# Kernel optimization log

Measured on AMD Instinct MI355X. Metric: run time of the kernel, lower is better.

The kernel has to match this reference:

```python
import jax, jax.numpy as jnp
import numpy as np

D_MODEL = 1024
N_HEADS = 16
HEAD_DIM = D_MODEL // N_HEADS


def setup_inputs() -> dict:
    key = jax.random.key(0)
    ks = jax.random.split(key, 5)
    s = 1.0 / np.sqrt(D_MODEL)
    return {
        "x": jax.random.normal(ks[0], (2, 2048, D_MODEL), dtype=jnp.float32),
        "w_qkv": jax.random.uniform(ks[1], (3 * D_MODEL, D_MODEL), jnp.float32, -s, s),
        "b_qkv": jax.random.uniform(ks[2], (3 * D_MODEL,), jnp.float32, -s, s),
        "w_out": jax.random.uniform(ks[3], (D_MODEL, D_MODEL), jnp.float32, -s, s),
        "b_out": jax.random.uniform(ks[4], (D_MODEL,), jnp.float32, -s, s),
    }


def _attn(x, w_qkv, b_qkv, w_out, b_out):
    bsz, seq_len, _ = x.shape
    qkv = jnp.einsum('bsd,ed->bse', x, w_qkv) + b_qkv  # [B,S,3D]
    q, k, v = jnp.split(qkv, 3, axis=-1)
    def heads(t):  # [B,S,D] -> [B,H,S,Dh]
        return t.reshape(bsz, seq_len, N_HEADS, HEAD_DIM).transpose(0, 2, 1, 3)
    q, k, v = heads(q), heads(k), heads(v)
    scores = jnp.einsum('bhqd,bhkd->bhqk', q, k) / np.sqrt(HEAD_DIM)
    mask = jnp.tril(jnp.ones((seq_len, seq_len), dtype=bool))
    scores = jnp.where(mask, scores, -jnp.inf)
    probs = jax.nn.softmax(scores, axis=-1)
    attn = jnp.einsum('bhqk,bhkd->bhqd', probs, v)
    attn = attn.transpose(0, 2, 1, 3).reshape(bsz, seq_len, D_MODEL)
    return jnp.einsum('bsd,ed->bse', attn, w_out) + b_out


def reference(x, w_qkv, b_qkv, w_out, b_out):
    return _attn(x, w_qkv, b_qkv, w_out, b_out)
```

## Files before the change

kernel.cpp:

```cpp
#include <hip/hip_runtime.h>
#include <hip/hip_bf16.h>
#include <stdint.h>

#define SEQ     2048
#define BATCH   2
#define NHEADS  16
#define HDIM    64
#define DMODEL  1024
#define N3      3072
#define D2      2048
#define MTOT    (BATCH*SEQ)

typedef __attribute__((ext_vector_type(4))) float f32x4;
typedef __attribute__((ext_vector_type(8))) short bf16x8;

static __device__ inline unsigned short f2bf(float f) {
    union { float f; unsigned u; } v; v.f = f;
    unsigned r = (v.u + 0x7fffu + ((v.u >> 16) & 1u)) >> 16;
    return (unsigned short)r;
}
static __device__ inline unsigned pk2bf(float a, float b) {
    union { __hip_bfloat162 h; unsigned u; } c;
    c.h = __float22bfloat162_rn(make_float2(a, b));
    return c.u;
}

#define GLDS(gp, lp) __builtin_amdgcn_global_load_lds( \
    (const __attribute__((address_space(1))) void*)(gp), \
    (__attribute__((address_space(3))) void*)(lp), 16, 0, 0)

__global__ void cast_all(const float* __restrict__ x,
                         const float* __restrict__ wqkv,
                         const float* __restrict__ wout,
                         unsigned short* __restrict__ xb,
                         unsigned short* __restrict__ wqkvb,
                         unsigned short* __restrict__ woutb) {
    long i4 = (long)(blockIdx.x * blockDim.x + threadIdx.x) * 4;
    const float* src; unsigned short* dst; long off;
    if (i4 < 4194304L)      { src = x;    dst = xb;    off = i4; }
    else if (i4 < 7340032L) { src = wqkv; dst = wqkvb; off = i4 - 4194304L; }
    else                    { src = wout; dst = woutb; off = i4 - 7340032L; }
    float4 v = *(const float4*)(src + off);
    union { uint2 u; ushort4 s; } pk;
    pk.u.x = pk2bf(v.x, v.y); pk.u.y = pk2bf(v.z, v.w);
    *(ushort4*)(dst + off) = pk.s;
}

__global__ __launch_bounds__(512, 1) void gemm_qkv(
    const unsigned short* __restrict__ A,
    const unsigned short* __restrict__ B,
    const float* __restrict__ bias,
    unsigned short* __restrict__ qk,
    unsigned short* __restrict__ vT)
{
    __shared__ __align__(16) unsigned short sA[2][256][64];
    __shared__ __align__(16) unsigned short sB[2][256][64];
    const int tid  = threadIdx.x;
    const int w    = tid >> 6, lane = tid & 63;
    const int quad = lane >> 4, l16 = lane & 15, l7 = l16 & 7;
    const int wm = w >> 2, wn = w & 3;
    const int bid = blockIdx.x;
    const int m0 = (bid & 15) << 8;
    const int n0 = (bid >> 4) << 8;

    f32x4 acc[8][4];
    const f32x4 zero = {0.f, 0.f, 0.f, 0.f};
    #pragma unroll
    for (int i = 0; i < 8; i++)
        #pragma unroll
        for (int j = 0; j < 4; j++) acc[i][j] = zero;

    const int rsel = tid >> 3;
    const int sgl  = (tid & 7) ^ (rsel & 7);
    const unsigned short* gA = A + (long)(m0 + rsel) * 1024 + sgl * 8;
    const unsigned short* gB = B + (long)(n0 + rsel) * 1024 + sgl * 8;
    const int srow = w * 8;

    bf16x8 af[4][2];
    bf16x8 bfr[2][2][2];

    auto stageA = [&](int nb, int h, long ko) {
        GLDS(gA + (long)(h * 128)      * 1024 + ko, &sA[nb][h * 128 +      srow][0]);
        GLDS(gA + (long)(h * 128 + 64) * 1024 + ko, &sA[nb][h * 128 + 64 + srow][0]);
    };
    auto stageB = [&](int nb, int h, long ko) {
        GLDS(gB + (long)(h * 128)      * 1024 + ko, &sB[nb][h * 128 +      srow][0]);
        GLDS(gB + (long)(h * 128 + 64) * 1024 + ko, &sB[nb][h * 128 + 64 + srow][0]);
    };
    auto loadA = [&](int c, int mh) {
        #pragma unroll
        for (int mt2 = 0; mt2 < 4; mt2++)
            #pragma unroll
            for (int kk = 0; kk < 2; kk++)
                af[mt2][kk] = *(const bf16x8*)(
                    &sA[c][mh * 128 + wm * 64 + mt2 * 16 + l16]
                          [(((kk << 2) + quad) ^ l7) * 8]);
    };
    auto loadB = [&](int c, int nh) {
        #pragma unroll
        for (int nt2 = 0; nt2 < 2; nt2++)
            #pragma unroll
            for (int kk = 0; kk < 2; kk++)
                bfr[nh][nt2][kk] = *(const bf16x8*)(
                    &sB[c][nh * 128 + wn * 32 + nt2 * 16 + l16]
                          [(((kk << 2) + quad) ^ l7) * 8]);
    };
    auto mfmaQ = [&](int mh, int nh) {
        __builtin_amdgcn_s_setprio(1);
        #pragma unroll
        for (int mt2 = 0; mt2 < 4; mt2++)
            #pragma unroll
            for (int nt2 = 0; nt2 < 2; nt2++)
                #pragma unroll
                for (int kk = 0; kk < 2; kk++)
                    acc[mh * 4 + mt2][nh * 2 + nt2] =
                        __builtin_amdgcn_mfma_f32_16x16x32_bf16(
                            af[mt2][kk], bfr[nh][nt2][kk],
                            acc[mh * 4 + mt2][nh * 2 + nt2], 0, 0, 0);
        __builtin_amdgcn_s_setprio(0);
    };

    stageB(0, 0, 0); stageB(0, 1, 0); stageA(0, 0, 0); stageA(0, 1, 0);
    __builtin_amdgcn_sched_barrier(0);
    asm volatile("s_waitcnt vmcnt(2)" ::: "memory");
    __builtin_amdgcn_sched_barrier(0);
    __builtin_amdgcn_s_barrier();

    for (int t = 0; t < 15; ++t) {
        const int c = t & 1, nb = c ^ 1;
        const long ko = (long)(t + 1) * 64;

        loadA(c, 0); loadB(c, 0);
        stageB(nb, 0, ko);
        __builtin_amdgcn_s_barrier();
        asm volatile("s_waitcnt lgkmcnt(0)" ::: "memory");
        __builtin_amdgcn_sched_barrier(0);
        mfmaQ(0, 0);
        __builtin_amdgcn_sched_barrier(0);
        __builtin_amdgcn_s_barrier();

        loadB(c, 1);
        stageB(nb, 1, ko);
        __builtin_amdgcn_sched_barrier(0);
        asm volatile("s_waitcnt vmcnt(4)" ::: "memory");
        __builtin_amdgcn_sched_barrier(0);
        __builtin_amdgcn_s_barrier();
        asm volatile("s_waitcnt lgkmcnt(0)" ::: "memory");
        __builtin_amdgcn_sched_barrier(0);
        mfmaQ(0, 1);
        __builtin_amdgcn_sched_barrier(0);
        __builtin_amdgcn_s_barrier();

        loadA(c, 1);
        stageA(nb, 0, ko);
        __builtin_amdgcn_s_barrier();
        asm volatile("s_waitcnt lgkmcnt(0)" ::: "memory");
        __builtin_amdgcn_sched_barrier(0);
        mfmaQ(1, 1);
        __builtin_amdgcn_sched_barrier(0);
        __builtin_amdgcn_s_barrier();

        stageA(nb, 1, ko);
        __builtin_amdgcn_sched_barrier(0);
        asm volatile("s_waitcnt vmcnt(2)" ::: "memory");
        __builtin_amdgcn_sched_barrier(0);
        __builtin_amdgcn_s_barrier();
        mfmaQ(1, 0);
        __builtin_amdgcn_sched_barrier(0);
        __builtin_amdgcn_s_barrier();
    }
    {
        const int c = 1;
        loadA(c, 0); loadB(c, 0);
        __builtin_amdgcn_s_barrier();
        asm volatile("s_waitcnt lgkmcnt(0)" ::: "memory");
        __builtin_amdgcn_sched_barrier(0);
        mfmaQ(0, 0);
        __builtin_amdgcn_sched_barrier(0);
        __builtin_amdgcn_s_barrier();

        loadB(c, 1);
        __builtin_amdgcn_sched_barrier(0);
        asm volatile("s_waitcnt vmcnt(0)" ::: "memory");
        __builtin_amdgcn_sched_barrier(0);
        __builtin_amdgcn_s_barrier();
        asm volatile("s_waitcnt lgkmcnt(0)" ::: "memory");
        __builtin_amdgcn_sched_barrier(0);
        mfmaQ(0, 1);
        __builtin_amdgcn_sched_barrier(0);
        __builtin_amdgcn_s_barrier();

        loadA(c, 1);
        __builtin_amdgcn_s_barrier();
        asm volatile("s_waitcnt lgkmcnt(0)" ::: "memory");
        __builtin_amdgcn_sched_barrier(0);
        mfmaQ(1, 1);
        mfmaQ(1, 0);
    }

    if (n0 < 2048) {
        #pragma unroll
        for (int ni = 0; ni < 4; ni++) {
            const int n_g = n0 + (ni >> 1) * 128 + wn * 32 + (ni & 1) * 16 + l16;
            const float bv = bias[n_g];
            #pragma unroll
            for (int mi = 0; mi < 8; mi++) {
                const int mb = (mi >> 2) * 128 + wm * 64 + (mi & 3) * 16 + quad * 4;
                #pragma unroll
                for (int r = 0; r < 4; r++) {
                    const int m_g = m0 + mb + r;
                    qk[(long)m_g * D2 + n_g] = f2bf(acc[mi][ni][r] + bv);
                }
            }
        }
    } else {
        const int b = m0 >> 11;
        #pragma unroll
        for (int ni = 0; ni < 4; ni++) {
            const int n_g = n0 + (ni >> 1) * 128 + wn * 32 + (ni & 1) * 16 + l16;
            const int dm = n_g - 2048;
            const long vrow = (long)(((b << 4) + (dm >> 6)) << 6) + (dm & 63);
            const float bv = bias[n_g];
            #pragma unroll
            for (int mi = 0; mi < 8; mi++) {
                const int m_g = m0 + (mi >> 2) * 128 + wm * 64 + (mi & 3) * 16 + quad * 4;
                union { uint2 u; ushort4 s; } pk;
                pk.u.x = pk2bf(acc[mi][ni][0] + bv, acc[mi][ni][1] + bv);
                pk.u.y = pk2bf(acc[mi][ni][2] + bv, acc[mi][ni][3] + bv);
                *(ushort4*)(vT + vrow * D2 + (m_g & 2047)) = pk.s;
            }
        }
    }
}

__global__ __launch_bounds__(256, 2) void gemm_out(
    const unsigned short* __restrict__ A,
    const unsigned short* __restrict__ B,
    const float* __restrict__ bias,
    float* __restrict__ C)
{
    __shared__ __align__(16) unsigned short sA[2][128][64];
    __shared__ __align__(16) unsigned short sB[2][64][64];
    const int tid  = threadIdx.x;
    const int wave = tid >> 6, lane = tid & 63;
    const int quad = lane >> 4, l16 = lane & 15, l7 = l16 & 7;
    const int wm = wave >> 1, wn = wave & 1;
    const int m0 = blockIdx.x * 128, n0 = blockIdx.y * 64;

    f32x4 acc[4][2];
    const f32x4 zero = {0.f, 0.f, 0.f, 0.f};
    #pragma unroll
    for (int i = 0; i < 4; i++) { acc[i][0] = zero; acc[i][1] = zero; }

    const int rsel = tid >> 3;
    const int sgl  = (tid & 7) ^ (rsel & 7);
    const unsigned short* gA0 = A + (long)(m0 + rsel) * 1024 + sgl * 8;
    const unsigned short* gB0 = B + (long)(n0 + rsel) * 1024 + sgl * 8;

    #pragma unroll
    for (int i = 0; i < 4; i++)
        GLDS(gA0 + (long)(32 * i) * 1024, &sA[0][32 * i + wave * 8][0]);
    #pragma unroll
    for (int i = 0; i < 2; i++)
        GLDS(gB0 + (long)(32 * i) * 1024, &sB[0][32 * i + wave * 8][0]);

    int buf = 0;
    for (int k0 = 0; k0 < 1024; k0 += 64, buf ^= 1) {
        __syncthreads();
        if (k0 + 64 < 1024) {
            #pragma unroll
            for (int i = 0; i < 4; i++)
                GLDS(gA0 + (long)(32 * i) * 1024 + k0 + 64, &sA[buf ^ 1][32 * i + wave * 8][0]);
            #pragma unroll
            for (int i = 0; i < 2; i++)
                GLDS(gB0 + (long)(32 * i) * 1024 + k0 + 64, &sB[buf ^ 1][32 * i + wave * 8][0]);
        }
        #pragma unroll
        for (int ks = 0; ks < 2; ks++) {
            bf16x8 af[4], bfr[2];
            #pragma unroll
            for (int mt = 0; mt < 4; mt++)
                af[mt] = *(const bf16x8*)(&sA[buf][wm * 64 + mt * 16 + l16][((ks * 4 + quad) ^ l7) * 8]);
            #pragma unroll
            for (int nt = 0; nt < 2; nt++)
                bfr[nt] = *(const bf16x8*)(&sB[buf][wn * 32 + nt * 16 + l16][((ks * 4 + quad) ^ l7) * 8]);
            #pragma unroll
            for (int mt = 0; mt < 4; mt++)
                #pragma unroll
                for (int nt = 0; nt < 2; nt++)
                    acc[mt][nt] = __builtin_amdgcn_mfma_f32_16x16x32_bf16(
                        af[mt], bfr[nt], acc[mt][nt], 0, 0, 0);
        }
    }
    #pragma unroll
    for (int nt = 0; nt < 2; nt++) {
        const int n_g = n0 + wn * 32 + nt * 16 + l16;
        const float bv = bias[n_g];
        #pragma unroll
        for (int mt = 0; mt < 4; mt++) {
            #pragma unroll
            for (int r = 0; r < 4; r++) {
                const int m_g = m0 + wm * 64 + mt * 16 + quad * 4 + r;
                C[(long)m_g * DMODEL + n_g] = acc[mt][nt][r] + bv;
            }
        }
    }
}

__global__ __launch_bounds__(512, 1) void attn_kernel(
    const unsigned short* __restrict__ qk,
    const unsigned short* __restrict__ vT,
    unsigned short* __restrict__ attn)
{
    __shared__ __align__(16) unsigned short sK [2][2][64][64];
    __shared__ __align__(16) unsigned short sVt[2][2][64][64];
    __shared__ __align__(16) unsigned short sP [8][16][64];

    const int tid  = threadIdx.x;
    const int w    = tid >> 6, lane = tid & 63;
    const int quad = lane >> 4, l16 = lane & 15, l7 = l16 & 7;

    const int bh = blockIdx.x;
    const int b  = bh >> 4, h = bh & 15;
    const int pair = blockIdx.y;
    const long rowb = (long)b * SEQ;

    const int rl = lane >> 3;
    const int sm = (lane & 7) ^ rl;
    const unsigned short* kg = qk + (rowb + w * 8 + rl) * D2 + 1024 + h * HDIM + sm * 8;
    const unsigned short* vg = vT + (long)(bh * 64 + w * 8 + rl) * D2 + sm * 8;

    const int s0 = quad ^ l7;
    const float C2 = 0.18033688011112042f;
    const f32x4 zero = {0.f, 0.f, 0.f, 0.f};

    #pragma unroll
    for (int ph = 0; ph < 2; ph++) {
        const int qtile  = ph ? (15 - pair) : pair;
        const int qbase  = qtile * 128;
        const int ntiles = 2 * qtile + 2;
        const int npairs = ntiles >> 1;

        bf16x8 qf0, qf1;
        {
            const unsigned short* qp = qk + (rowb + qbase + w * 16 + l16) * D2 + h * HDIM;
            qf0 = *(const bf16x8*)(qp + quad * 8);
            qf1 = *(const bf16x8*)(qp + 32 + quad * 8);
        }
        f32x4 Oacc[4];
        #pragma unroll
        for (int mf = 0; mf < 4; mf++) Oacc[mf] = zero;
        float l_i = 0.f;

        __syncthreads();
        {
            GLDS(kg,            &sK [0][0][w * 8][0]);
            GLDS(vg,            &sVt[0][0][w * 8][0]);
            GLDS(kg + 64L * D2, &sK [0][1][w * 8][0]);
            GLDS(vg + 64,       &sVt[0][1][w * 8][0]);
        }

        int buf = 0;
        for (int p = 0; p < npairs; p++, buf ^= 1) {
            __syncthreads();
            if (p + 1 < npairs) {
                const long o0 = (long)(2 * p + 2) * 64;
                const long o1 = (long)(2 * p + 3) * 64;
                GLDS(kg + o0 * D2, &sK [buf ^ 1][0][w * 8][0]);
                GLDS(vg + o0,      &sVt[buf ^ 1][0][w * 8][0]);
                GLDS(kg + o1 * D2, &sK [buf ^ 1][1][w * 8][0]);
                GLDS(vg + o1,      &sVt[buf ^ 1][1][w * 8][0]);
            }
            #pragma unroll
            for (int s = 0; s < 2; s++) {
                const int t = 2 * p + s;

                f32x4 st[4];
                __builtin_amdgcn_s_setprio(1);
                #pragma unroll
                for (int kvf = 0; kvf < 4; kvf++) {
                    bf16x8 kf0 = *(const bf16x8*)(&sK[buf][s][kvf * 16 + l16][s0 * 8]);
                    bf16x8 kf1 = *(const bf16x8*)(&sK[buf][s][kvf * 16 + l16][(s0 ^ 4) * 8]);
                    st[kvf] = __builtin_amdgcn_mfma_f32_16x16x32_bf16(kf0, qf0, zero, 0, 0, 0);
                    st[kvf] = __builtin_amdgcn_mfma_f32_16x16x32_bf16(kf1, qf1, st[kvf], 0, 0, 0);
                }
                __builtin_amdgcn_s_setprio(0);
                if (t >= 2 * qtile) {
                    const int ql = w * 16 + l16;
                    const int tb = (t - 2 * qtile) * 64;
                    #pragma unroll
                    for (int kvf = 0; kvf < 4; kvf++) {
                        const int kv = tb + kvf * 16 + quad * 4;
                        #pragma unroll
                        for (int r = 0; r < 4; r++)
                            if (kv + r > ql) st[kvf][r] = -1e30f;
                    }
                }
                #pragma unroll
                for (int kvf = 0; kvf < 4; kvf++) {
                    #pragma unroll
                    for (int r = 0; r < 4; r++)
                        st[kvf][r] = __builtin_amdgcn_exp2f(st[kvf][r] * C2);
                }
                f32x4 ps = (st[0] + st[1]) + (st[2] + st[3]);
                l_i += (ps[0] + ps[1]) + (ps[2] + ps[3]);

                #pragma unroll
                for (int kvf = 0; kvf < 4; kvf++) {
                    union { uint2 u; ushort4 s4; } pk;
                    pk.u.x = pk2bf(st[kvf][0], st[kvf][1]);
                    pk.u.y = pk2bf(st[kvf][2], st[kvf][3]);
                    const int seg = (kvf * 2 + (quad >> 1)) ^ l7;
                    *(ushort4*)(&sP[w][l16][seg * 8 + (quad & 1) * 4]) = pk.s4;
                }
                bf16x8 pf0 = *(const bf16x8*)(&sP[w][l16][(quad ^ l7) * 8]);
                bf16x8 pf1 = *(const bf16x8*)(&sP[w][l16][((4 + quad) ^ l7) * 8]);
                __builtin_amdgcn_s_setprio(1);
                #pragma unroll
                for (int mf = 0; mf < 4; mf++) {
                    bf16x8 vf0 = *(const bf16x8*)(&sVt[buf][s][mf * 16 + l16][s0 * 8]);
                    bf16x8 vf1 = *(const bf16x8*)(&sVt[buf][s][mf * 16 + l16][(s0 ^ 4) * 8]);
                    Oacc[mf] = __builtin_amdgcn_mfma_f32_16x16x32_bf16(vf0, pf0, Oacc[mf], 0, 0, 0);
                    Oacc[mf] = __builtin_amdgcn_mfma_f32_16x16x32_bf16(vf1, pf1, Oacc[mf], 0, 0, 0);
                }
                __builtin_amdgcn_s_setprio(0);
            }
        }
        float L = l_i;
        L += __shfl_xor(L, 16);
        L += __shfl_xor(L, 32);
        const float inv = 1.0f / L;
        const int q = qbase + w * 16 + l16;
        unsigned short* op = attn + (rowb + q) * DMODEL + h * HDIM + quad * 4;
        #pragma unroll
        for (int mf = 0; mf < 4; mf++) {
            union { uint2 u; ushort4 s4; } pk;
            pk.u.x = pk2bf(Oacc[mf][0] * inv, Oacc[mf][1] * inv);
            pk.u.y = pk2bf(Oacc[mf][2] * inv, Oacc[mf][3] * inv);
            *(ushort4*)(op + mf * 16) = pk.s4;
        }
    }
}

extern "C" void kernel_launch(void* const* d_in, const int* in_sizes, int n_in,
                              void* d_out, int out_size, void* d_ws, size_t ws_size,
                              hipStream_t stream) {
    const float* x    = (const float*)d_in[0];
    const float* wqkv = (const float*)d_in[1];
    const float* bqkv = (const float*)d_in[2];
    const float* wout = (const float*)d_in[3];
    const float* bout = (const float*)d_in[4];

    char* ws = (char*)d_ws;
    unsigned short* xb    = (unsigned short*)(ws);
    unsigned short* wqkvb = (unsigned short*)(ws + (8L << 20));
    unsigned short* woutb = (unsigned short*)(ws + (14L << 20));
    unsigned short* qkb   = (unsigned short*)(ws + (16L << 20));
    unsigned short* vTb   = (unsigned short*)(ws + (32L << 20));
    unsigned short* attnb = (unsigned short*)(ws + (40L << 20));

    cast_all<<<8192, 256, 0, stream>>>(x, wqkv, wout, xb, wqkvb, woutb);

    gemm_qkv<<<192, 512, 0, stream>>>(xb, wqkvb, bqkv, qkb, vTb);

    dim3 g2(32, 8);
    attn_kernel<<<g2, 512, 0, stream>>>(qkb, vTb, attnb);

    dim3 g3(32, 16);
    gemm_out<<<g3, 256, 0, stream>>>(attnb, woutb, bout, (float*)d_out);
}
```

Measured before the change: 171.4 us.

## Fuse cast, QKV GEMM, attention and output GEMM into one cooperative kernel

```diff
diff --git a/kernel.cpp b/kernel.cpp
--- a/kernel.cpp
+++ b/kernel.cpp
@@ -1,6 +1,9 @@
 #include <hip/hip_runtime.h>
 #include <hip/hip_bf16.h>
+#include <hip/hip_cooperative_groups.h>
 #include <stdint.h>
+
+namespace cg = cooperative_groups;
 
 #define SEQ     2048
 #define BATCH   2
@@ -29,415 +32,411 @@
     (const __attribute__((address_space(1))) void*)(gp), \
     (__attribute__((address_space(3))) void*)(lp), 16, 0, 0)
 
-__global__ void cast_all(const float* __restrict__ x,
-                         const float* __restrict__ wqkv,
-                         const float* __restrict__ wout,
-                         unsigned short* __restrict__ xb,
-                         unsigned short* __restrict__ wqkvb,
-                         unsigned short* __restrict__ woutb) {
-    long i4 = (long)(blockIdx.x * blockDim.x + threadIdx.x) * 4;
-    const float* src; unsigned short* dst; long off;
-    if (i4 < 4194304L)      { src = x;    dst = xb;    off = i4; }
-    else if (i4 < 7340032L) { src = wqkv; dst = wqkvb; off = i4 - 4194304L; }
-    else                    { src = wout; dst = woutb; off = i4 - 7340032L; }
-    float4 v = *(const float4*)(src + off);
-    union { uint2 u; ushort4 s; } pk;
-    pk.u.x = pk2bf(v.x, v.y); pk.u.y = pk2bf(v.z, v.w);
-    *(ushort4*)(dst + off) = pk.s;
-}
-
-__global__ __launch_bounds__(512, 1) void gemm_qkv(
-    const unsigned short* __restrict__ A,
-    const unsigned short* __restrict__ B,
-    const float* __restrict__ bias,
+__global__ __launch_bounds__(512, 1) void fused(
+    const float* __restrict__ x,
+    const float* __restrict__ wqkv,
+    const float* __restrict__ bqkv,
+    const float* __restrict__ wout,
+    const float* __restrict__ bout,
+    unsigned short* __restrict__ xb,
+    unsigned short* __restrict__ wqkvb,
+    unsigned short* __restrict__ woutb,
     unsigned short* __restrict__ qk,
-    unsigned short* __restrict__ vT)
+    unsigned short* __restrict__ vT,
+    unsigned short* __restrict__ attnb,
+    float* __restrict__ out)
 {
-    __shared__ __align__(16) unsigned short sA[2][256][64];
-    __shared__ __align__(16) unsigned short sB[2][256][64];
-    const int tid  = threadIdx.x;
+    __shared__ __align__(16) char smem[131072];
+    const int vb  = blockIdx.x;
+    const int tid = threadIdx.x;
     const int w    = tid >> 6, lane = tid & 63;
     const int quad = lane >> 4, l16 = lane & 15, l7 = l16 & 7;
-    const int wm = w >> 2, wn = w & 3;
-    const int bid = blockIdx.x;
-    const int m0 = (bid & 15) << 8;
-    const int n0 = (bid >> 4) << 8;
-
-    f32x4 acc[8][4];
+    cg::grid_group grid = cg::this_grid();
     const f32x4 zero = {0.f, 0.f, 0.f, 0.f};
-    #pragma unroll
-    for (int i = 0; i < 8; i++)
+
+    {
+        const long gid = (long)vb * 512 + tid;
+        for (int p = 0; p < 16; p++) {
+            long i4 = (p * 131072L + gid) * 4;
+            const float* src; unsigned short* dst; long off;
+            if (i4 < 4194304L)      { src = x;    dst = xb;    off = i4; }
+            else if (i4 < 7340032L) { src = wqkv; dst = wqkvb; off = i4 - 4194304L; }
+            else                    { src = wout; dst = woutb; off = i4 - 7340032L; }
+            float4 v = *(const float4*)(src + off);
+            union { uint2 u; ushort4 s; } pk;
+            pk.u.x = pk2bf(v.x, v.y); pk.u.y = pk2bf(v.z, v.w);
+            *(ushort4*)(dst + off) = pk.s;
+        }
+    }
+    __threadfence();
+    grid.sync();
+
+    if (vb < 192) {
+        unsigned short (*sA)[256][64] = (unsigned short (*)[256][64])(smem);
+        unsigned short (*sB)[256][64] = (unsigned short (*)[256][64])(smem + 65536);
+        const int wm = w >> 2, wn = w & 3;
+        const int m0 = (vb & 15) << 8;
+        const int n0 = (vb >> 4) << 8;
+
+        f32x4 acc[8][4];
         #pragma unroll
-        for (int j = 0; j < 4; j++) acc[i][j] = zero;
-
-    const int rsel = tid >> 3;
-    const int sgl  = (tid & 7) ^ (rsel & 7);
-    const unsigned short* gA = A + (long)(m0 + rsel) * 1024 + sgl * 8;
-    const unsigned short* gB = B + (long)(n0 + rsel) * 1024 + sgl * 8;
-    const int srow = w * 8;
-
-    bf16x8 af[4][2];
-    bf16x8 bfr[2][2][2];
-
-    auto stageA = [&](int nb, int h, long ko) {
-        GLDS(gA + (long)(h * 128)      * 1024 + ko, &sA[nb][h * 128 +      srow][0]);
-        GLDS(gA + (long)(h * 128 + 64) * 1024 + ko, &sA[nb][h * 128 + 64 + srow][0]);
-    };
-    auto stageB = [&](int nb, int h, long ko) {
-        GLDS(gB + (long)(h * 128)      * 1024 + ko, &sB[nb][h * 128 +      srow][0]);
-        GLDS(gB + (long)(h * 128 + 64) * 1024 + ko, &sB[nb][h * 128 + 64 + srow][0]);
-    };
-    auto loadA = [&](int c, int mh) {
-        #pragma unroll
-        for (int mt2 = 0; mt2 < 4; mt2++)
-            #pragma unroll
-            for (int kk = 0; kk < 2; kk++)
-                af[mt2][kk] = *(const bf16x8*)(
-                    &sA[c][mh * 128 + wm * 64 + mt2 * 16 + l16]
-                          [(((kk << 2) + quad) ^ l7) * 8]);
-    };
-    auto loadB = [&](int c, int nh) {
-        #pragma unroll
-        for (int nt2 = 0; nt2 < 2; nt2++)
-            #pragma unroll
-            for (int kk = 0; kk < 2; kk++)
-                bfr[nh][nt2][kk] = *(const bf16x8*)(
-                    &sB[c][nh * 128 + wn * 32 + nt2 * 16 + l16]
-                          [(((kk << 2) + quad) ^ l7) * 8]);
-    };
-    auto mfmaQ = [&](int mh, int nh) {
-        __builtin_amdgcn_s_setprio(1);
-        #pragma unroll
-        for (int mt2 = 0; mt2 < 4; mt2++)
+        for (int i = 0; i < 8; i++)
+            #pragma unroll
+            for (int j = 0; j < 4; j++) acc[i][j] = zero;
+
+        const int rsel = tid >> 3;
+        const int sgl  = (tid & 7) ^ (rsel & 7);
+        const unsigned short* gA = xb    + (long)(m0 + rsel) * 1024 + sgl * 8;
+        const unsigned short* gB = wqkvb + (long)(n0 + rsel) * 1024 + sgl * 8;
+        const int srow = w * 8;
+
+        bf16x8 af[4][2];
+        bf16x8 bfr[2][2][2];
+
+        auto stageA = [&](int nb, int h, long ko) {
+            GLDS(gA + (long)(h * 128)      * 1024 + ko, &sA[nb][h * 128 +      srow][0]);
+            GLDS(gA + (long)(h * 128 + 64) * 1024 + ko, &sA[nb][h * 128 + 64 + srow][0]);
+        };
+        auto stageB = [&](int nb, int h, long ko) {
+            GLDS(gB + (long)(h * 128)      * 1024 + ko, &sB[nb][h * 128 +      srow][0]);
+            GLDS(gB + (long)(h * 128 + 64) * 1024 + ko, &sB[nb][h * 128 + 64 + srow][0]);
+        };
+        auto loadA = [&](int c, int mh) {
+            #pragma unroll
+            for (int mt2 = 0; mt2 < 4; mt2++)
+                #pragma unroll
+                for (int kk = 0; kk < 2; kk++)
+                    af[mt2][kk] = *(const bf16x8*)(
+                        &sA[c][mh * 128 + wm * 64 + mt2 * 16 + l16]
+                              [(((kk << 2) + quad) ^ l7) * 8]);
+        };
+        auto loadB = [&](int c, int nh) {
             #pragma unroll
             for (int nt2 = 0; nt2 < 2; nt2++)
                 #pragma unroll
                 for (int kk = 0; kk < 2; kk++)
-                    acc[mh * 4 + mt2][nh * 2 + nt2] =
-                        __builtin_amdgcn_mfma_f32_16x16x32_bf16(
-                            af[mt2][kk], bfr[nh][nt2][kk],
-                            acc[mh * 4 + mt2][nh * 2 + nt2], 0, 0, 0);
-        __builtin_amdgcn_s_setprio(0);
-    };
-
-    stageB(0, 0, 0); stageB(0, 1, 0); stageA(0, 0, 0); stageA(0, 1, 0);
-    __builtin_amdgcn_sched_barrier(0);
-    asm volatile("s_waitcnt vmcnt(2)" ::: "memory");
-    __builtin_amdgcn_sched_barrier(0);
-    __builtin_amdgcn_s_barrier();
-
-    for (int t = 0; t < 15; ++t) {
-        const int c = t & 1, nb = c ^ 1;
-        const long ko = (long)(t + 1) * 64;
-
-        loadA(c, 0); loadB(c, 0);
-        stageB(nb, 0, ko);
-        __builtin_amdgcn_s_barrier();
-        asm volatile("s_waitcnt lgkmcnt(0)" ::: "memory");
-        __builtin_amdgcn_sched_barrier(0);
-        mfmaQ(0, 0);
-        __builtin_amdgcn_sched_barrier(0);
-        __builtin_amdgcn_s_barrier();
-
-        loadB(c, 1);
-        stageB(nb, 1, ko);
-        __builtin_amdgcn_sched_barrier(0);
-        asm volatile("s_waitcnt vmcnt(4)" ::: "memory");
-        __builtin_amdgcn_sched_barrier(0);
-        __builtin_amdgcn_s_barrier();
-        asm volatile("s_waitcnt lgkmcnt(0)" ::: "memory");
-        __builtin_amdgcn_sched_barrier(0);
-        mfmaQ(0, 1);
-        __builtin_amdgcn_sched_barrier(0);
-        __builtin_amdgcn_s_barrier();
-
-        loadA(c, 1);
-        stageA(nb, 0, ko);
-        __builtin_amdgcn_s_barrier();
-        asm volatile("s_waitcnt lgkmcnt(0)" ::: "memory");
-        __builtin_amdgcn_sched_barrier(0);
-        mfmaQ(1, 1);
-        __builtin_amdgcn_sched_barrier(0);
-        __builtin_amdgcn_s_barrier();
-
-        stageA(nb, 1, ko);
+                    bfr[nh][nt2][kk] = *(const bf16x8*)(
+                        &sB[c][nh * 128 + wn * 32 + nt2 * 16 + l16]
+                              [(((kk << 2) + quad) ^ l7) * 8]);
+        };
+        auto mfmaQ = [&](int mh, int nh) {
+            __builtin_amdgcn_s_setprio(1);
+            #pragma unroll
+            for (int mt2 = 0; mt2 < 4; mt2++)
+                #pragma unroll
+                for (int nt2 = 0; nt2 < 2; nt2++)
+                    #pragma unroll
+                    for (int kk = 0; kk < 2; kk++)
+                        acc[mh * 4 + mt2][nh * 2 + nt2] =
+                            __builtin_amdgcn_mfma_f32_16x16x32_bf16(
+                                af[mt2][kk], bfr[nh][nt2][kk],
+                                acc[mh * 4 + mt2][nh * 2 + nt2], 0, 0, 0);
+            __builtin_amdgcn_s_setprio(0);
+        };
+
+        stageB(0, 0, 0); stageB(0, 1, 0); stageA(0, 0, 0); stageA(0, 1, 0);
         __builtin_amdgcn_sched_barrier(0);
         asm volatile("s_waitcnt vmcnt(2)" ::: "memory");
         __builtin_amdgcn_sched_barrier(0);
         __builtin_amdgcn_s_barrier();
-        mfmaQ(1, 0);
-        __builtin_amdgcn_sched_barrier(0);
-        __builtin_amdgcn_s_barrier();
+
+        for (int t = 0; t < 15; ++t) {
+            const int c = t & 1, nb = c ^ 1;
+            const long ko = (long)(t + 1) * 64;
+
+            loadA(c, 0); loadB(c, 0);
+            stageB(nb, 0, ko);
+            __builtin_amdgcn_s_barrier();
+            asm volatile("s_waitcnt lgkmcnt(0)" ::: "memory");
+            __builtin_amdgcn_sched_barrier(0);
+            mfmaQ(0, 0);
+            __builtin_amdgcn_sched_barrier(0);
+            __builtin_amdgcn_s_barrier();
+
+            loadB(c, 1);
+            stageB(nb, 1, ko);
+            __builtin_amdgcn_sched_barrier(0);
+            asm volatile("s_waitcnt vmcnt(4)" ::: "memory");
+            __builtin_amdgcn_sched_barrier(0);
+            __builtin_amdgcn_s_barrier();
+            asm volatile("s_waitcnt lgkmcnt(0)" ::: "memory");
+            __builtin_amdgcn_sched_barrier(0);
+            mfmaQ(0, 1);
+            __builtin_amdgcn_sched_barrier(0);
+            __builtin_amdgcn_s_barrier();
+
+            loadA(c, 1);
+            stageA(nb, 0, ko);
+            __builtin_amdgcn_s_barrier();
+            asm volatile("s_waitcnt lgkmcnt(0)" ::: "memory");
+            __builtin_amdgcn_sched_barrier(0);
+            mfmaQ(1, 1);
+            __builtin_amdgcn_sched_barrier(0);
+            __builtin_amdgcn_s_barrier();
+
+            stageA(nb, 1, ko);
+            __builtin_amdgcn_sched_barrier(0);
+            asm volatile("s_waitcnt vmcnt(2)" ::: "memory");
+            __builtin_amdgcn_sched_barrier(0);
+            __builtin_amdgcn_s_barrier();
+            mfmaQ(1, 0);
+            __builtin_amdgcn_sched_barrier(0);
+            __builtin_amdgcn_s_barrier();
+        }
+        {
+            const int c = 1;
+            loadA(c, 0); loadB(c, 0);
+            __builtin_amdgcn_s_barrier();
+            asm volatile("s_waitcnt lgkmcnt(0)" ::: "memory");
+            __builtin_amdgcn_sched_barrier(0);
+            mfmaQ(0, 0);
+            __builtin_amdgcn_sched_barrier(0);
+            __builtin_amdgcn_s_barrier();
+
+            loadB(c, 1);
+            __builtin_amdgcn_sched_barrier(0);
+            asm volatile("s_waitcnt vmcnt(0)" ::: "memory");
+            __builtin_amdgcn_sched_barrier(0);
+            __builtin_amdgcn_s_barrier();
+            asm volatile("s_waitcnt lgkmcnt(0)" ::: "memory");
+            __builtin_amdgcn_sched_barrier(0);
+            mfmaQ(0, 1);
+            __builtin_amdgcn_sched_barrier(0);
+            __builtin_amdgcn_s_barrier();
+
+            loadA(c, 1);
+            __builtin_amdgcn_s_barrier();
+            asm volatile("s_waitcnt lgkmcnt(0)" ::: "memory");
+            __builtin_amdgcn_sched_barrier(0);
+            mfmaQ(1, 1);
+            mfmaQ(1, 0);
+        }
+
+        if (n0 < 2048) {
+            #pragma unroll
+            for (int ni = 0; ni < 4; ni++) {
+                const int n_g = n0 + (ni >> 1) * 128 + wn * 32 + (ni & 1) * 16 + l16;
+                const float bv = bqkv[n_g];
+                #pragma unroll
+                for (int mi = 0; mi < 8; mi++) {
+                    const int mb = (mi >> 2) * 128 + wm * 64 + (mi & 3) * 16 + quad * 4;
+                    #pragma unroll
+                    for (int r = 0; r < 4; r++) {
+                        const int m_g = m0 + mb + r;
+                        qk[(long)m_g * D2 + n_g] = f2bf(acc[mi][ni][r] + bv);
+                    }
+                }
+            }
+        } else {
+            const int b = m0 >> 11;
+            #pragma unroll
+            for (int ni = 0; ni < 4; ni++) {
+                const int n_g = n0 + (ni >> 1) * 128 + wn * 32 + (ni & 1) * 16 + l16;
+                const int dm = n_g - 2048;
+                const long vrow = (long)(((b << 4) + (dm >> 6)) << 6) + (dm & 63);
+                const float bv = bqkv[n_g];
+                #pragma unroll
+                for (int mi = 0; mi < 8; mi++) {
+                    const int m_g = m0 + (mi >> 2) * 128 + wm * 64 + (mi & 3) * 16 + quad * 4;
+                    union { uint2 u; ushort4 s; } pk;
+                    pk.u.x = pk2bf(acc[mi][ni][0] + bv, acc[mi][ni][1] + bv);
+                    pk.u.y = pk2bf(acc[mi][ni][2] + bv, acc[mi][ni][3] + bv);
+                    *(ushort4*)(vT + vrow * D2 + (m_g & 2047)) = pk.s;
+                }
+            }
+        }
     }
+    __threadfence();
+    grid.sync();
+
     {
-        const int c = 1;
-        loadA(c, 0); loadB(c, 0);
-        __builtin_amdgcn_s_barrier();
-        asm volatile("s_waitcnt lgkmcnt(0)" ::: "memory");
-        __builtin_amdgcn_sched_barrier(0);
-        mfmaQ(0, 0);
-        __builtin_amdgcn_sched_barrier(0);
-        __builtin_amdgcn_s_barrier();
-
-        loadB(c, 1);
-        __builtin_amdgcn_sched_barrier(0);
-        asm volatile("s_waitcnt vmcnt(0)" ::: "memory");
-        __builtin_amdgcn_sched_barrier(0);
-        __builtin_amdgcn_s_barrier();
-        asm volatile("s_waitcnt lgkmcnt(0)" ::: "memory");
-        __builtin_amdgcn_sched_barrier(0);
-        mfmaQ(0, 1);
-        __builtin_amdgcn_sched_barrier(0);
-        __builtin_amdgcn_s_barrier();
-
-        loadA(c, 1);
-        __builtin_amdgcn_s_barrier();
-        asm volatile("s_waitcnt lgkmcnt(0)" ::: "memory");
-        __builtin_amdgcn_sched_barrier(0);
-        mfmaQ(1, 1);
-        mfmaQ(1, 0);
-    }
-
-    if (n0 < 2048) {
+        unsigned short (*sK)[2][64][64]  = (unsigned short (*)[2][64][64])(smem);
+        unsigned short (*sVt)[2][64][64] = (unsigned short (*)[2][64][64])(smem + 32768);
+        unsigned short (*sP)[16][64]     = (unsigned short (*)[16][64])(smem + 65536);
+
+        const int bh = vb >> 3;
+        const int b  = bh >> 4, h = bh & 15;
+        const int pair = vb & 7;
+        const long rowb = (long)b * SEQ;
+
+        const int rl = lane >> 3;
+        const int sm = (lane & 7) ^ rl;
+        const unsigned short* kg = qk + (rowb + w * 8 + rl) * D2 + 1024 + h * HDIM + sm * 8;
+        const unsigned short* vg = vT + (long)(bh * 64 + w * 8 + rl) * D2 + sm * 8;
+
+        const int s0 = quad ^ l7;
+        const float C2 = 0.18033688011112042f;
+
         #pragma unroll
-        for (int ni = 0; ni < 4; ni++) {
-            const int n_g = n0 + (ni >> 1) * 128 + wn * 32 + (ni & 1) * 16 + l16;
-            const float bv = bias[n_g];
-            #pragma unroll
-            for (int mi = 0; mi < 8; mi++) {
-                const int mb = (mi >> 2) * 128 + wm * 64 + (mi & 3) * 16 + quad * 4;
-                #pragma unroll
-                for (int r = 0; r < 4; r++) {
-                    const int m_g = m0 + mb + r;
-                    qk[(long)m_g * D2 + n_g] = f2bf(acc[mi][ni][r] + bv);
+        for (int ph = 0; ph < 2; ph++) {
+            const int qtile  = ph ? (15 - pair) : pair;
+            const int qbase  = qtile * 128;
+            const int ntiles = 2 * qtile + 2;
+            const int npairs = ntiles >> 1;
+
+            bf16x8 qf0, qf1;
+            {
+                const unsigned short* qp = qk + (rowb + qbase + w * 16 + l16) * D2 + h * HDIM;
+                qf0 = *(const bf16x8*)(qp + quad * 8);
+                qf1 = *(const bf16x8*)(qp + 32 + quad * 8);
+            }
+            f32x4 Oacc[4];
+            #pragma unroll
+            for (int mf = 0; mf < 4; mf++) Oacc[mf] = zero;
+            float l_i = 0.f;
+
+            __syncthreads();
+            {
+                GLDS(kg,            &sK [0][0][w * 8][0]);
+                GLDS(vg,            &sVt[0][0][w * 8][0]);
+                GLDS(kg + 64L * D2, &sK [0][1][w * 8][0]);
+                GLDS(vg + 64,       &sVt[0][1][w * 8][0]);
+            }
+
+            int buf = 0;
+            for (int p = 0; p < npairs; p++, buf ^= 1) {
+                __syncthreads();
+                if (p + 1 < npairs) {
+                    const long o0 = (long)(2 * p + 2) * 64;
+                    const long o1 = (long)(2 * p + 3) * 64;
+                    GLDS(kg + o0 * D2, &sK [buf ^ 1][0][w * 8][0]);
+                    GLDS(vg + o0,      &sVt[buf ^ 1][0][w * 8][0]);
+                    GLDS(kg + o1 * D2, &sK [buf ^ 1][1][w * 8][0]);
+                    GLDS(vg + o1,      &sVt[buf ^ 1][1][w * 8][0]);
                 }
-            }
-        }
-    } else {
-        const int b = m0 >> 11;
-        #pragma unroll
-        for (int ni = 0; ni < 4; ni++) {
-            const int n_g = n0 + (ni >> 1) * 128 + wn * 32 + (ni & 1) * 16 + l16;
-            const int dm = n_g - 2048;
-            const long vrow = (long)(((b << 4) + (dm >> 6)) << 6) + (dm & 63);
-            const float bv = bias[n_g];
-            #pragma unroll
-            for (int mi = 0; mi < 8; mi++) {
-                const int m_g = m0 + (mi >> 2) * 128 + wm * 64 + (mi & 3) * 16 + quad * 4;
-                union { uint2 u; ushort4 s; } pk;
-                pk.u.x = pk2bf(acc[mi][ni][0] + bv, acc[mi][ni][1] + bv);
-                pk.u.y = pk2bf(acc[mi][ni][2] + bv, acc[mi][ni][3] + bv);
-                *(ushort4*)(vT + vrow * D2 + (m_g & 2047)) = pk.s;
-            }
-        }
-    }
-}
-
-__global__ __launch_bounds__(256, 2) void gemm_out(
-    const unsigned short* __restrict__ A,
-    const unsigned short* __restrict__ B,
-    const float* __restrict__ bias,
-    float* __restrict__ C)
-{
-    __shared__ __align__(16) unsigned short sA[2][128][64];
-    __shared__ __align__(16) unsigned short sB[2][64][64];
-    const int tid  = threadIdx.x;
-    const int wave = tid >> 6, lane = tid & 63;
-    const int quad = lane >> 4, l16 = lane & 15, l7 = l16 & 7;
-    const int wm = wave >> 1, wn = wave & 1;
-    const int m0 = blockIdx.x * 128, n0 = blockIdx.y * 64;
-
-    f32x4 acc[4][2];
-    const f32x4 zero = {0.f, 0.f, 0.f, 0.f};
-    #pragma unroll
-    for (int i = 0; i < 4; i++) { acc[i][0] = zero; acc[i][1] = zero; }
-
-    const int rsel = tid >> 3;
-    const int sgl  = (tid & 7) ^ (rsel & 7);
-    const unsigned short* gA0 = A + (long)(m0 + rsel) * 1024 + sgl * 8;
-    const unsigned short* gB0 = B + (long)(n0 + rsel) * 1024 + sgl * 8;
-
-    #pragma unroll
-    for (int i = 0; i < 4; i++)
-        GLDS(gA0 + (long)(32 * i) * 1024, &sA[0][32 * i + wave * 8][0]);
-    #pragma unroll
-    for (int i = 0; i < 2; i++)
-        GLDS(gB0 + (long)(32 * i) * 1024, &sB[0][32 * i + wave * 8][0]);
-
-    int buf = 0;
-    for (int k0 = 0; k0 < 1024; k0 += 64, buf ^= 1) {
-        __syncthreads();
-        if (k0 + 64 < 1024) {
-            #pragma unroll
-            for (int i = 0; i < 4; i++)
-                GLDS(gA0 + (long)(32 * i) * 1024 + k0 + 64, &sA[buf ^ 1][32 * i + wave * 8][0]);
-            #pragma unroll
-            for (int i = 0; i < 2; i++)
-                GLDS(gB0 + (long)(32 * i) * 1024 + k0 + 64, &sB[buf ^ 1][32 * i + wave * 8][0]);
-        }
-        #pragma unroll
-        for (int ks = 0; ks < 2; ks++) {
-            bf16x8 af[4], bfr[2];
-            #pragma unroll
-            for (int mt = 0; mt < 4; mt++)
-                af[mt] = *(const bf16x8*)(&sA[buf][wm * 64 + mt * 16 + l16][((ks * 4 + quad) ^ l7) * 8]);
-            #pragma unroll
-            for (int nt = 0; nt < 2; nt++)
-                bfr[nt] = *(const bf16x8*)(&sB[buf][wn * 32 + nt * 16 + l16][((ks * 4 + quad) ^ l7) * 8]);
-            #pragma unroll
-            for (int mt = 0; mt < 4; mt++)
-                #pragma unroll
-                for (int nt = 0; nt < 2; nt++)
-                    acc[mt][nt] = __builtin_amdgcn_mfma_f32_16x16x32_bf16(
-                        af[mt], bfr[nt], acc[mt][nt], 0, 0, 0);
-        }
-    }
-    #pragma unroll
-    for (int nt = 0; nt < 2; nt++) {
-        const int n_g = n0 + wn * 32 + nt * 16 + l16;
-        const float bv = bias[n_g];
-        #pragma unroll
-        for (int mt = 0; mt < 4; mt++) {
-            #pragma unroll
-            for (int r = 0; r < 4; r++) {
-                const int m_g = m0 + wm * 64 + mt * 16 + quad * 4 + r;
-                C[(long)m_g * DMODEL + n_g] = acc[mt][nt][r] + bv;
-            }
-        }
-    }
-}
-
-__global__ __launch_bounds__(512, 1) void attn_kernel(
-    const unsigned short* __restrict__ qk,
-    const unsigned short* __restrict__ vT,
-    unsigned short* __restrict__ attn)
-{
-    __shared__ __align__(16) unsigned short sK [2][2][64][64];
-    __shared__ __align__(16) unsigned short sVt[2][2][64][64];
-    __shared__ __align__(16) unsigned short sP [8][16][64];
-
-    const int tid  = threadIdx.x;
-    const int w    = tid >> 6, lane = tid & 63;
-    const int quad = lane >> 4, l16 = lane & 15, l7 = l16 & 7;
-
-    const int bh = blockIdx.x;
-    const int b  = bh >> 4, h = bh & 15;
-    const int pair = blockIdx.y;
-    const long rowb = (long)b * SEQ;
-
-    const int rl = lane >> 3;
-    const int sm = (lane & 7) ^ rl;
-    const unsigned short* kg = qk + (rowb + w * 8 + rl) * D2 + 1024 + h * HDIM + sm * 8;
-    const unsigned short* vg = vT + (long)(bh * 64 + w * 8 + rl) * D2 + sm * 8;
-
-    const int s0 = quad ^ l7;
-    const float C2 = 0.18033688011112042f;
-    const f32x4 zero = {0.f, 0.f, 0.f, 0.f};
-
-    #pragma unroll
-    for (int ph = 0; ph < 2; ph++) {
-        const int qtile  = ph ? (15 - pair) : pair;
-        const int qbase  = qtile * 128;
-        const int ntiles = 2 * qtile + 2;
-        const int npairs = ntiles >> 1;
-
-        bf16x8 qf0, qf1;
-        {
-            const unsigned short* qp = qk + (rowb + qbase + w * 16 + l16) * D2 + h * HDIM;
-            qf0 = *(const bf16x8*)(qp + quad * 8);
-            qf1 = *(const bf16x8*)(qp + 32 + quad * 8);
-        }
-        f32x4 Oacc[4];
-        #pragma unroll
-        for (int mf = 0; mf < 4; mf++) Oacc[mf] = zero;
-        float l_i = 0.f;
-
-        __syncthreads();
-        {
-            GLDS(kg,            &sK [0][0][w * 8][0]);
-            GLDS(vg,            &sVt[0][0][w * 8][0]);
-            GLDS(kg + 64L * D2, &sK [0][1][w * 8][0]);
-            GLDS(vg + 64,       &sVt[0][1][w * 8][0]);
-        }
-
-        int buf = 0;
-        for (int p = 0; p < npairs; p++, buf ^= 1) {
-            __syncthreads();
-            if (p + 1 < npairs) {
-                const long o0 = (long)(2 * p + 2) * 64;
-                const long o1 = (long)(2 * p + 3) * 64;
-                GLDS(kg + o0 * D2, &sK [buf ^ 1][0][w * 8][0]);
-                GLDS(vg + o0,      &sVt[buf ^ 1][0][w * 8][0]);
-                GLDS(kg + o1 * D2, &sK [buf ^ 1][1][w * 8][0]);
-                GLDS(vg + o1,      &sVt[buf ^ 1][1][w * 8][0]);
-            }
-            #pragma unroll
-            for (int s = 0; s < 2; s++) {
-                const int t = 2 * p + s;
-
-                f32x4 st[4];
-                __builtin_amdgcn_s_setprio(1);
-                #pragma unroll
-                for (int kvf = 0; kvf < 4; kvf++) {
-                    bf16x8 kf0 = *(const bf16x8*)(&sK[buf][s][kvf * 16 + l16][s0 * 8]);
-                    bf16x8 kf1 = *(const bf16x8*)(&sK[buf][s][kvf * 16 + l16][(s0 ^ 4) * 8]);
-                    st[kvf] = __builtin_amdgcn_mfma_f32_16x16x32_bf16(kf0, qf0, zero, 0, 0, 0);
-                    st[kvf] = __builtin_amdgcn_mfma_f32_16x16x32_bf16(kf1, qf1, st[kvf], 0, 0, 0);
-                }
-                __builtin_amdgcn_s_setprio(0);
-                if (t >= 2 * qtile) {
-                    const int ql = w * 16 + l16;
-                    const int tb = (t - 2 * qtile) * 64;
+                #pragma unroll
+                for (int s = 0; s < 2; s++) {
+                    const int t = 2 * p + s;
+
+                    f32x4 st[4];
+                    __builtin_amdgcn_s_setprio(1);
                     #pragma unroll
                     for (int kvf = 0; kvf < 4; kvf++) {
-                        const int kv = tb + kvf * 16 + quad * 4;
+                        bf16x8 kf0 = *(const bf16x8*)(&sK[buf][s][kvf * 16 + l16][s0 * 8]);
+                        bf16x8 kf1 = *(const bf16x8*)(&sK[buf][s][kvf * 16 + l16][(s0 ^ 4) * 8]);
+                        st[kvf] = __builtin_amdgcn_mfma_f32_16x16x32_bf16(kf0, qf0, zero, 0, 0, 0);
+                        st[kvf] = __builtin_amdgcn_mfma_f32_16x16x32_bf16(kf1, qf1, st[kvf], 0, 0, 0);
+                    }
+                    __builtin_amdgcn_s_setprio(0);
+                    if (t >= 2 * qtile) {
+                        const int ql = w * 16 + l16;
+                        const int tb = (t - 2 * qtile) * 64;
+                        #pragma unroll
+                        for (int kvf = 0; kvf < 4; kvf++) {
+                            const int kv = tb + kvf * 16 + quad * 4;
+                            #pragma unroll
+                            for (int r = 0; r < 4; r++)
+                                if (kv + r > ql) st[kvf][r] = -1e30f;
+                        }
+                    }
+                    #pragma unroll
+                    for (int kvf = 0; kvf < 4; kvf++) {
                         #pragma unroll
                         for (int r = 0; r < 4; r++)
-                            if (kv + r > ql) st[kvf][r] = -1e30f;
-                    }
+                            st[kvf][r] = __builtin_amdgcn_exp2f(st[kvf][r] * C2);
+                    }
+                    f32x4 ps = (st[0] + st[1]) + (st[2] + st[3]);
+                    l_i += (ps[0] + ps[1]) + (ps[2] + ps[3]);
+
+                    #pragma unroll
+                    for (int kvf = 0; kvf < 4; kvf++) {
+                        union { uint2 u; ushort4 s4; } pk;
+                        pk.u.x = pk2bf(st[kvf][0], st[kvf][1]);
+                        pk.u.y = pk2bf(st[kvf][2], st[kvf][3]);
+                        const int seg = (kvf * 2 + (quad >> 1)) ^ l7;
+                        *(ushort4*)(&sP[w][l16][seg * 8 + (quad & 1) * 4]) = pk.s4;
+                    }
+                    bf16x8 pf0 = *(const bf16x8*)(&sP[w][l16][(quad ^ l7) * 8]);
+                    bf16x8 pf1 = *(const bf16x8*)(&sP[w][l16][((4 + quad) ^ l7) * 8]);
+                    __builtin_amdgcn_s_setprio(1);
+                    #pragma unroll
+                    for (int mf = 0; mf < 4; mf++) {
+                        bf16x8 vf0 = *(const bf16x8*)(&sVt[buf][s][mf * 16 + l16][s0 * 8]);
+                        bf16x8 vf1 = *(const bf16x8*)(&sVt[buf][s][mf * 16 + l16][(s0 ^ 4) * 8]);
+                        Oacc[mf] = __builtin_amdgcn_mfma_f32_16x16x32_bf16(vf0, pf0, Oacc[mf], 0, 0, 0);
+                        Oacc[mf] = __builtin_amdgcn_mfma_f32_16x16x32_bf16(vf1, pf1, Oacc[mf], 0, 0, 0);
+                    }
+                    __builtin_amdgcn_s_setprio(0);
                 }
-                #pragma unroll
-                for (int kvf = 0; kvf < 4; kvf++) {
-                    #pragma unroll
-                    for (int r = 0; r < 4; r++)
-                        st[kvf][r] = __builtin_amdgcn_exp2f(st[kvf][r] * C2);
+            }
+            float L = l_i;
+            L += __shfl_xor(L, 16);
+            L += __shfl_xor(L, 32);
+            const float inv = 1.0f / L;
+            const int q = qbase + w * 16 + l16;
+            unsigned short* op = attnb + (rowb + q) * DMODEL + h * HDIM + quad * 4;
+            #pragma unroll
+            for (int mf = 0; mf < 4; mf++) {
+                union { uint2 u; ushort4 s4; } pk;
+                pk.u.x = pk2bf(Oacc[mf][0] * inv, Oacc[mf][1] * inv);
+                pk.u.y = pk2bf(Oacc[mf][2] * inv, Oacc[mf][3] * inv);
+                *(ushort4*)(op + mf * 16) = pk.s4;
+            }
+        }
+    }
+    __threadfence();
+    grid.sync();
+
+    {
+        unsigned short (*sA)[128][64] = (unsigned short (*)[128][64])(smem);
+        unsigned short (*sB)[128][64] = (unsigned short (*)[128][64])(smem + 65536);
+        const int wm = w >> 2, wn = w & 3;
+        const int m0 = (vb >> 3) * 128;
+        const int n0 = (vb & 7) * 128;
+
+        f32x4 acc[4][2];
+        #pragma unroll
+        for (int i = 0; i < 4; i++) { acc[i][0] = zero; acc[i][1] = zero; }
+
+        const int rsel = tid >> 3;
+        const int sgl  = (tid & 7) ^ (rsel & 7);
+        const unsigned short* gA0 = attnb + (long)(m0 + rsel) * 1024 + sgl * 8;
+        const unsigned short* gB0 = woutb + (long)(n0 + rsel) * 1024 + sgl * 8;
+        const int srow = w * 8;
+
+        GLDS(gA0,               &sA[0][srow][0]);
+        GLDS(gA0 + 64L * 1024,  &sA[0][64 + srow][0]);
+        GLDS(gB0,               &sB[0][srow][0]);
+        GLDS(gB0 + 64L * 1024,  &sB[0][64 + srow][0]);
+
+        int buf = 0;
+        for (int k0 = 0; k0 < 1024; k0 += 64, buf ^= 1) {
+            __syncthreads();
+            if (k0 + 64 < 1024) {
+                GLDS(gA0 + k0 + 64,              &sA[buf ^ 1][srow][0]);
+                GLDS(gA0 + 64L * 1024 + k0 + 64, &sA[buf ^ 1][64 + srow][0]);
+                GLDS(gB0 + k0 + 64,              &sB[buf ^ 1][srow][0]);
+                GLDS(gB0 + 64L * 1024 + k0 + 64, &sB[buf ^ 1][64 + srow][0]);
+            }
+            #pragma unroll
+            for (int ks = 0; ks < 2; ks++) {
+                bf16x8 af[4], bfr[2];
+                #pragma unroll
+                for (int mt = 0; mt < 4; mt++)
+                    af[mt] = *(const bf16x8*)(&sA[buf][wm * 64 + mt * 16 + l16][((ks * 4 + quad) ^ l7) * 8]);
+                #pragma unroll
+                for (int nt = 0; nt < 2; nt++)
+                    bfr[nt] = *(const bf16x8*)(&sB[buf][wn * 32 + nt * 16 + l16][((ks * 4 + quad) ^ l7) * 8]);
+                #pragma unroll
+                for (int mt = 0; mt < 4; mt++)
+                    #pragma unroll
+                    for (int nt = 0; nt < 2; nt++)
+                        acc[mt][nt] = __builtin_amdgcn_mfma_f32_16x16x32_bf16(
+                            af[mt], bfr[nt], acc[mt][nt], 0, 0, 0);
+            }
+        }
+        #pragma unroll
+        for (int nt = 0; nt < 2; nt++) {
+            const int n_g = n0 + wn * 32 + nt * 16 + l16;
+            const float bv = bout[n_g];
+            #pragma unroll
+            for (int mt = 0; mt < 4; mt++) {
+                #pragma unroll
+                for (int r = 0; r < 4; r++) {
+                    const int m_g = m0 + wm * 64 + mt * 16 + quad * 4 + r;
+                    out[(long)m_g * DMODEL + n_g] = acc[mt][nt][r] + bv;
                 }
-                f32x4 ps = (st[0] + st[1]) + (st[2] + st[3]);
-                l_i += (ps[0] + ps[1]) + (ps[2] + ps[3]);
-
-                #pragma unroll
-                for (int kvf = 0; kvf < 4; kvf++) {
-                    union { uint2 u; ushort4 s4; } pk;
-                    pk.u.x = pk2bf(st[kvf][0], st[kvf][1]);
-                    pk.u.y = pk2bf(st[kvf][2], st[kvf][3]);
-                    const int seg = (kvf * 2 + (quad >> 1)) ^ l7;
-                    *(ushort4*)(&sP[w][l16][seg * 8 + (quad & 1) * 4]) = pk.s4;
-                }
-                bf16x8 pf0 = *(const bf16x8*)(&sP[w][l16][(quad ^ l7) * 8]);
-                bf16x8 pf1 = *(const bf16x8*)(&sP[w][l16][((4 + quad) ^ l7) * 8]);
-                __builtin_amdgcn_s_setprio(1);
-                #pragma unroll
-                for (int mf = 0; mf < 4; mf++) {
-                    bf16x8 vf0 = *(const bf16x8*)(&sVt[buf][s][mf * 16 + l16][s0 * 8]);
-                    bf16x8 vf1 = *(const bf16x8*)(&sVt[buf][s][mf * 16 + l16][(s0 ^ 4) * 8]);
-                    Oacc[mf] = __builtin_amdgcn_mfma_f32_16x16x32_bf16(vf0, pf0, Oacc[mf], 0, 0, 0);
-                    Oacc[mf] = __builtin_amdgcn_mfma_f32_16x16x32_bf16(vf1, pf1, Oacc[mf], 0, 0, 0);
-                }
-                __builtin_amdgcn_s_setprio(0);
-            }
-        }
-        float L = l_i;
-        L += __shfl_xor(L, 16);
-        L += __shfl_xor(L, 32);
-        const float inv = 1.0f / L;
-        const int q = qbase + w * 16 + l16;
-        unsigned short* op = attn + (rowb + q) * DMODEL + h * HDIM + quad * 4;
-        #pragma unroll
-        for (int mf = 0; mf < 4; mf++) {
-            union { uint2 u; ushort4 s4; } pk;
-            pk.u.x = pk2bf(Oacc[mf][0] * inv, Oacc[mf][1] * inv);
-            pk.u.y = pk2bf(Oacc[mf][2] * inv, Oacc[mf][3] * inv);
-            *(ushort4*)(op + mf * 16) = pk.s4;
+            }
         }
     }
 }
@@ -458,14 +457,13 @@
     unsigned short* qkb   = (unsigned short*)(ws + (16L << 20));
     unsigned short* vTb   = (unsigned short*)(ws + (32L << 20));
     unsigned short* attnb = (unsigned short*)(ws + (40L << 20));
-
-    cast_all<<<8192, 256, 0, stream>>>(x, wqkv, wout, xb, wqkvb, woutb);
-
-    gemm_qkv<<<192, 512, 0, stream>>>(xb, wqkvb, bqkv, qkb, vTb);
-
-    dim3 g2(32, 8);
-    attn_kernel<<<g2, 512, 0, stream>>>(qkb, vTb, attnb);
-
-    dim3 g3(32, 16);
-    gemm_out<<<g3, 256, 0, stream>>>(attnb, woutb, bout, (float*)d_out);
+    float*          outp  = (float*)d_out;
+
+    void* args[] = {
+        (void*)&x, (void*)&wqkv, (void*)&bqkv, (void*)&wout, (void*)&bout,
+        (void*)&xb, (void*)&wqkvb, (void*)&woutb,
+        (void*)&qkb, (void*)&vTb, (void*)&attnb, (void*)&outp
+    };
+    hipLaunchCooperativeKernel((const void*)fused, dim3(256), dim3(512),
+                               args, 0, stream);
 }
```

After: 446.1 us. 160% more time.
